# Performance work log

Hardware: AMD Instinct MI355X
Metric: run time of the kernel (lower is better)

The kernel has to match this reference:

```python
import jax, jax.numpy as jnp
import numpy as np

EMBED_DIM = 1024
NUM_HEADS = 16
HEAD_DIM = EMBED_DIM // NUM_HEADS
B, S = 2, 2048


def setup_inputs() -> dict:
    key = jax.random.key(0)
    ks = jax.random.split(key, 11)
    init = 0.02
    return {
        "query": jax.random.normal(ks[0], (B, S, EMBED_DIM), jnp.float32),
        "key": jax.random.normal(ks[1], (B, S, EMBED_DIM), jnp.float32),
        "value": jax.random.normal(ks[2], (B, S, EMBED_DIM), jnp.float32),
        "Wq": jax.random.normal(ks[3], (EMBED_DIM, EMBED_DIM), jnp.float32) * init,
        "bq": jnp.zeros((EMBED_DIM,), jnp.float32),
        "Wk": jax.random.normal(ks[4], (EMBED_DIM, EMBED_DIM), jnp.float32) * init,
        "bk": jnp.zeros((EMBED_DIM,), jnp.float32),
        "Wv": jax.random.normal(ks[5], (EMBED_DIM, EMBED_DIM), jnp.float32) * init,
        "bv": jnp.zeros((EMBED_DIM,), jnp.float32),
        "Wo": jax.random.normal(ks[6], (EMBED_DIM, EMBED_DIM), jnp.float32) * init,
        "bo": jnp.zeros((EMBED_DIM,), jnp.float32),
    }


def reference(query, key, value, Wq, bq, Wk, bk, Wv, bv, Wo, bo):
    scale = jnp.sqrt(jnp.asarray(HEAD_DIM, query.dtype))
    # projections (torch Linear: x @ W.T + b)
    Q = query @ Wq.T + bq
    K = key @ Wk.T + bk
    V = value @ Wv.T + bv
    # [B, S, E] -> [B, H, S, D]
    def split_heads(x):
        return x.reshape(B, -1, NUM_HEADS, HEAD_DIM).transpose(0, 2, 1, 3)
    Qh, Kh, Vh = split_heads(Q), split_heads(K), split_heads(V)
    # scores: [B, H, S, S] -- the O(N^2) intermediate
    scores = jnp.einsum("bhqd,bhkd->bhqk", Qh, Kh) / scale
    attn_weights = jax.nn.softmax(scores, axis=-1)
    # dropout = 0.0 (eval mode)
    out = jnp.einsum("bhqk,bhkd->bhqd", attn_weights, Vh)
    out = out.transpose(0, 2, 1, 3).reshape(B, -1, EMBED_DIM)
    output = out @ Wo.T + bo
    return output, attn_weights
```

## Files before the change

### kernel.cpp

```cpp
#include <hip/hip_runtime.h>
#include <hip/hip_bf16.h>

typedef unsigned short u16;
typedef u16 u16x8 __attribute__((ext_vector_type(8)));
typedef u16 u16x4 __attribute__((ext_vector_type(4)));
typedef __bf16 bf16x8 __attribute__((ext_vector_type(8)));
typedef float f32x4 __attribute__((ext_vector_type(4)));

#define B_ 2
#define S_ 2048
#define E_ 1024
#define H_ 16
#define D_ 64
#define QSCALE 0.18033688011112042f

__device__ __forceinline__ u16 f2bf(float f) {
    return __builtin_bit_cast(u16, static_cast<__bf16>(f));
}
__device__ __forceinline__ float bf2f(unsigned u) {
    return __builtin_bit_cast(float, u << 16);
}

__device__ __forceinline__ void glds16(const u16* g, u16* l) {
    __builtin_amdgcn_global_load_lds(
        (const __attribute__((address_space(1))) unsigned int*)g,
        (__attribute__((address_space(3))) unsigned int*)l, 16, 0, 0);
}

#define VMCNT0 asm volatile("s_waitcnt vmcnt(0)" ::: "memory")
#define RAW_BAR() do { __builtin_amdgcn_s_barrier(); asm volatile("" ::: "memory"); } while (0)

__device__ __forceinline__ bf16x8 lds_read8(const u16* base, int row, int k) {
    const char* p = (const char*)base + (((row * 128) + (k * 2)) ^ ((row & 7) << 4));
    return __builtin_bit_cast(bf16x8, *(const u16x8*)p);
}

__device__ __forceinline__ f32x4 mfma16x16(bf16x8 a, bf16x8 b, f32x4 c) {
    return __builtin_amdgcn_mfma_f32_16x16x32_bf16(a, b, c, 0, 0, 0);
}

__global__ __launch_bounds__(256) void cvt_kernel(const float* __restrict__ q,
                                                  const float* __restrict__ k,
                                                  const float* __restrict__ v,
                                                  const float* __restrict__ wq,
                                                  const float* __restrict__ wk,
                                                  const float* __restrict__ wv,
                                                  const float* __restrict__ wo,
                                                  u16* __restrict__ qkv_dst,
                                                  u16* __restrict__ w_dst) {
    const int bid = blockIdx.x;
    const float* src;
    u16* dst;
    if (bid < 6144) {
        const int t = bid >> 11, lb = bid & 2047;
        src = (t == 0 ? q : t == 1 ? k : v) + (size_t)lb * 2048;
        dst = qkv_dst + (size_t)t * 4194304 + (size_t)lb * 2048;
    } else {
        const int t = (bid - 6144) >> 9, lb = (bid - 6144) & 511;
        src = (t == 0 ? wq : t == 1 ? wk : t == 2 ? wv : wo) + (size_t)lb * 2048;
        dst = w_dst + (size_t)t * 1048576 + (size_t)lb * 2048;
    }
    const int off = threadIdx.x * 8;
    f32x4 a = *(const f32x4*)(src + off);
    f32x4 b = *(const f32x4*)(src + off + 4);
    u16x8 o;
#pragma unroll
    for (int i = 0; i < 4; ++i) { o[i] = f2bf(a[i]); o[4 + i] = f2bf(b[i]); }
    *(u16x8*)(dst + off) = o;
}

__global__ __launch_bounds__(256) void gemm_qkv(const u16* __restrict__ qkv_bf,
                                                const u16* __restrict__ w_bf,
                                                const float* __restrict__ bq,
                                                const float* __restrict__ bk,
                                                const float* __restrict__ bv,
                                                u16* __restrict__ outbase) {
    const int z = blockIdx.z;
    const u16* A = qkv_bf + (size_t)z * 4194304;
    const u16* W = w_bf + (size_t)z * 1048576;
    const float* bias = (z == 0) ? bq : (z == 1) ? bk : bv;
    u16* outp = outbase + (size_t)z * 4194304;

    const int n0 = blockIdx.x * 64;
    const int m0 = blockIdx.y * 128;
    const int tid = threadIdx.x;
    const int lane = tid & 63, g = lane >> 4, c = lane & 15;
    const int w = tid >> 6, wm = w >> 1, wn = w & 1;

    __shared__ u16 lA[2][8192];
    __shared__ u16 lB[2][4096];

    auto stage = [&](int buf, int kt) {
#pragma unroll
        for (int i = 0; i < 4; ++i) {
            const int chunk = (w * 4 + i) * 64 + lane;
            const int r = chunk >> 3, sg = chunk & 7, ss = sg ^ (r & 7);
            glds16(A + (size_t)(m0 + r) * 1024 + kt * 64 + ss * 8, &lA[buf][(w * 4 + i) * 512]);
        }
#pragma unroll
        for (int i = 0; i < 2; ++i) {
            const int chunk = (w * 2 + i) * 64 + lane;
            const int r = chunk >> 3, sg = chunk & 7, ss = sg ^ (r & 7);
            glds16(W + (size_t)(n0 + r) * 1024 + kt * 64 + ss * 8, &lB[buf][(w * 2 + i) * 512]);
        }
    };

    f32x4 acc[4][2] = {};
    stage(0, 0);
    VMCNT0;
    __syncthreads();

    for (int kt = 0; kt < 16; ++kt) {
        const int buf = kt & 1;
        if (kt < 15) stage(buf ^ 1, kt + 1);
#pragma unroll
        for (int ks = 0; ks < 2; ++ks) {
            bf16x8 af[4], bfr[2];
#pragma unroll
            for (int fm = 0; fm < 4; ++fm) af[fm] = lds_read8(lA[buf], wm * 64 + fm * 16 + c, g * 8 + ks * 32);
#pragma unroll
            for (int fn = 0; fn < 2; ++fn) bfr[fn] = lds_read8(lB[buf], wn * 32 + fn * 16 + c, g * 8 + ks * 32);
#pragma unroll
            for (int fm = 0; fm < 4; ++fm)
#pragma unroll
                for (int fn = 0; fn < 2; ++fn)
                    acc[fm][fn] = mfma16x16(af[fm], bfr[fn], acc[fm][fn]);
        }
        VMCNT0;
        RAW_BAR();
    }

    float bv_[2];
#pragma unroll
    for (int fn = 0; fn < 2; ++fn) bv_[fn] = bias[n0 + wn * 32 + fn * 16 + c];

#pragma unroll
    for (int fm = 0; fm < 4; ++fm) {
#pragma unroll
        for (int fn = 0; fn < 2; ++fn) {
            const int mbase = m0 + wm * 64 + fm * 16 + g * 4;
            const int n = n0 + wn * 32 + fn * 16 + c;
            if (z == 2) {
                u16x4 vv;
#pragma unroll
                for (int r = 0; r < 4; ++r) vv[r] = f2bf(acc[fm][fn][r] + bv_[fn]);
                const int b = mbase >> 11, s = mbase & 2047, h = n >> 6, d = n & 63;
                u16* dst = outp + ((size_t)((b * 16 + h) * 64 + d)) * 2048 + s;
                *(u16x4*)dst = vv;
            } else {
                const float sc = (z == 0) ? QSCALE : 1.0f;
#pragma unroll
                for (int r = 0; r < 4; ++r) {
                    const float val = (acc[fm][fn][r] + bv_[fn]) * sc;
                    const int m = mbase + r;
                    const int b = m >> 11, s = m & 2047, h = n >> 6, d = n & 63;
                    outp[((size_t)((b * 16 + h) * 2048 + s)) * 64 + d] = f2bf(val);
                }
            }
        }
    }
}

__global__ __launch_bounds__(256) void gemm_out(const u16* __restrict__ A,
                                                const u16* __restrict__ W,
                                                const float* __restrict__ bias,
                                                float* __restrict__ outp) {
    const int n0 = blockIdx.x * 64;
    const int m0 = blockIdx.y * 128;
    const int tid = threadIdx.x;
    const int lane = tid & 63, g = lane >> 4, c = lane & 15;
    const int w = tid >> 6, wm = w >> 1, wn = w & 1;

    __shared__ u16 lA[2][8192];
    __shared__ u16 lB[2][4096];

    auto stage = [&](int buf, int kt) {
#pragma unroll
        for (int i = 0; i < 4; ++i) {
            const int chunk = (w * 4 + i) * 64 + lane;
            const int r = chunk >> 3, sg = chunk & 7, ss = sg ^ (r & 7);
            glds16(A + (size_t)(m0 + r) * 1024 + kt * 64 + ss * 8, &lA[buf][(w * 4 + i) * 512]);
        }
#pragma unroll
        for (int i = 0; i < 2; ++i) {
            const int chunk = (w * 2 + i) * 64 + lane;
            const int r = chunk >> 3, sg = chunk & 7, ss = sg ^ (r & 7);
            glds16(W + (size_t)(n0 + r) * 1024 + kt * 64 + ss * 8, &lB[buf][(w * 2 + i) * 512]);
        }
    };

    f32x4 acc[4][2] = {};
    stage(0, 0);
    VMCNT0;
    __syncthreads();

    for (int kt = 0; kt < 16; ++kt) {
        const int buf = kt & 1;
        if (kt < 15) stage(buf ^ 1, kt + 1);
#pragma unroll
        for (int ks = 0; ks < 2; ++ks) {
            bf16x8 af[4], bfr[2];
#pragma unroll
            for (int fm = 0; fm < 4; ++fm) af[fm] = lds_read8(lA[buf], wm * 64 + fm * 16 + c, g * 8 + ks * 32);
#pragma unroll
            for (int fn = 0; fn < 2; ++fn) bfr[fn] = lds_read8(lB[buf], wn * 32 + fn * 16 + c, g * 8 + ks * 32);
#pragma unroll
            for (int fm = 0; fm < 4; ++fm)
#pragma unroll
                for (int fn = 0; fn < 2; ++fn)
                    acc[fm][fn] = mfma16x16(af[fm], bfr[fn], acc[fm][fn]);
        }
        VMCNT0;
        RAW_BAR();
    }

    float bv_[2];
#pragma unroll
    for (int fn = 0; fn < 2; ++fn) bv_[fn] = bias[n0 + wn * 32 + fn * 16 + c];

#pragma unroll
    for (int fm = 0; fm < 4; ++fm)
#pragma unroll
        for (int fn = 0; fn < 2; ++fn) {
            const int mbase = m0 + wm * 64 + fm * 16 + g * 4;
            const int n = n0 + wn * 32 + fn * 16 + c;
#pragma unroll
            for (int r = 0; r < 4; ++r)
                outp[(size_t)(mbase + r) * 1024 + n] = acc[fm][fn][r] + bv_[fn];
        }
}

__global__ __launch_bounds__(256) void attn_kernel(const u16* __restrict__ Qh,
                                                   const u16* __restrict__ Kh,
                                                   const u16* __restrict__ Vt,
                                                   float* __restrict__ attnW,
                                                   u16* __restrict__ Obf) {
    const int bid = blockIdx.x;
    const int sw = ((bid & 7) << 6) + (bid >> 3);
    const int bh = sw >> 4, qt = sw & 15;
    const int tid = threadIdx.x;
    const int lane = tid & 63, g = lane >> 4, c = lane & 15;
    const int w = tid >> 6;

    __shared__ u16 lQ[8192];
    __shared__ u16 lK[2][4096];
    __shared__ u16 lV[2][4096];
    __shared__ u16 lP[4][2048];

    const u16* Qbase = Qh + ((size_t)bh * S_ + qt * 128) * D_;
    const u16* Kbase = Kh + (size_t)bh * S_ * D_;
    const u16* Vbase = Vt + (size_t)bh * D_ * S_;

#pragma unroll
    for (int i = 0; i < 4; ++i) {
        const int chunk = (w * 4 + i) * 64 + lane;
        const int r = chunk >> 3, sg = chunk & 7, ss = sg ^ (r & 7);
        glds16(Qbase + r * 64 + ss * 8, &lQ[(w * 4 + i) * 512]);
    }
    auto stageK = [&](int buf, int kt) {
#pragma unroll
        for (int i = 0; i < 2; ++i) {
            const int chunk = (w * 2 + i) * 64 + lane;
            const int r = chunk >> 3, sg = chunk & 7, ss = sg ^ (r & 7);
            glds16(Kbase + (size_t)(kt * 64 + r) * 64 + ss * 8, &lK[buf][(w * 2 + i) * 512]);
        }
    };
    auto stageV = [&](int buf, int kt) {
#pragma unroll
        for (int i = 0; i < 2; ++i) {
            const int chunk = (w * 2 + i) * 64 + lane;
            const int r = chunk >> 3, sg = chunk & 7, ss = sg ^ (r & 7);
            glds16(Vbase + (size_t)r * S_ + kt * 64 + ss * 8, &lV[buf][(w * 2 + i) * 512]);
        }
    };

    stageK(0, 0);
    VMCNT0;
    __syncthreads();

    float l_run[2] = {0.f, 0.f};

    for (int kt = 0; kt < 32; ++kt) {
        const int buf = kt & 1;
        if (kt < 31) stageK(buf ^ 1, kt + 1);

        f32x4 s[4][2] = {};
        __builtin_amdgcn_s_setprio(1);
#pragma unroll
        for (int ks = 0; ks < 2; ++ks) {
            bf16x8 a[4], b[2];
#pragma unroll
            for (int kf = 0; kf < 4; ++kf) a[kf] = lds_read8(lK[buf], kf * 16 + c, g * 8 + ks * 32);
#pragma unroll
            for (int qf = 0; qf < 2; ++qf) b[qf] = lds_read8(lQ, w * 32 + qf * 16 + c, g * 8 + ks * 32);
#pragma unroll
            for (int kf = 0; kf < 4; ++kf)
#pragma unroll
                for (int qf = 0; qf < 2; ++qf)
                    s[kf][qf] = mfma16x16(a[kf], b[qf], s[kf][qf]);
        }
        __builtin_amdgcn_s_setprio(0);
#pragma unroll
        for (int qf = 0; qf < 2; ++qf) {
            float ts = 0.f;
#pragma unroll
            for (int kf = 0; kf < 4; ++kf)
#pragma unroll
                for (int r = 0; r < 4; ++r) ts += exp2f(s[kf][qf][r]);
            ts += __shfl_xor(ts, 16);
            ts += __shfl_xor(ts, 32);
            l_run[qf] += ts;
        }
        VMCNT0;
        RAW_BAR();
    }
    const float linv[2] = {1.f / l_run[0], 1.f / l_run[1]};

    f32x4 o[2][4] = {};
    stageK(0, 0);
    stageV(0, 0);
    VMCNT0;
    __syncthreads();

    for (int kt = 0; kt < 32; ++kt) {
        const int buf = kt & 1;
        if (kt < 31) { stageK(buf ^ 1, kt + 1); stageV(buf ^ 1, kt + 1); }

        f32x4 s[4][2] = {};
        __builtin_amdgcn_s_setprio(1);
#pragma unroll
        for (int ks = 0; ks < 2; ++ks) {
            bf16x8 a[4], b[2];
#pragma unroll
            for (int kf = 0; kf < 4; ++kf) a[kf] = lds_read8(lK[buf], kf * 16 + c, g * 8 + ks * 32);
#pragma unroll
            for (int qf = 0; qf < 2; ++qf) b[qf] = lds_read8(lQ, w * 32 + qf * 16 + c, g * 8 + ks * 32);
#pragma unroll
            for (int kf = 0; kf < 4; ++kf)
#pragma unroll
                for (int qf = 0; qf < 2; ++qf)
                    s[kf][qf] = mfma16x16(a[kf], b[qf], s[kf][qf]);
        }
        __builtin_amdgcn_s_setprio(0);

        u16* myP = lP[w];
#pragma unroll
        for (int qf = 0; qf < 2; ++qf) {
#pragma unroll
            for (int kf = 0; kf < 4; ++kf) {
                f32x4 p4;
#pragma unroll
                for (int r = 0; r < 4; ++r) p4[r] = exp2f(s[kf][qf][r]) * linv[qf];
#pragma unroll
                for (int rp = 0; rp < 2; ++rp) {
                    const unsigned pk = (unsigned)f2bf(p4[2 * rp]) |
                                        ((unsigned)f2bf(p4[2 * rp + 1]) << 16);
                    const int row = qf * 16 + c;
                    const int col = kf * 16 + g * 4 + 2 * rp;
                    *(unsigned*)((char*)myP + (((row * 128) + (col * 2)) ^ ((row & 7) << 4))) = pk;
                }
            }
        }

        __builtin_amdgcn_s_setprio(1);
#pragma unroll
        for (int ks = 0; ks < 2; ++ks) {
            bf16x8 pa[2], vb[4];
#pragma unroll
            for (int fm = 0; fm < 2; ++fm) pa[fm] = lds_read8(myP, fm * 16 + c, g * 8 + ks * 32);
#pragma unroll
            for (int fn = 0; fn < 4; ++fn) vb[fn] = lds_read8(lV[buf], fn * 16 + c, g * 8 + ks * 32);
#pragma unroll
            for (int fm = 0; fm < 2; ++fm)
#pragma unroll
                for (int fn = 0; fn < 4; ++fn)
                    o[fm][fn] = mfma16x16(pa[fm], vb[fn], o[fm][fn]);
        }
        __builtin_amdgcn_s_setprio(0);

        {
            const size_t qbase = (size_t)bh * S_ + (size_t)(qt * 128 + w * 32);
#pragma unroll
            for (int j = 0; j < 8; ++j) {
                const int row = j * 4 + g;
                const unsigned long long pv8 = *(const unsigned long long*)(
                    (const char*)myP + (((row * 128) + c * 8) ^ ((row & 7) << 4)));
                f32x4 o4;
                o4[0] = bf2f((unsigned)(pv8 & 0xffffu));
                o4[1] = bf2f((unsigned)((pv8 >> 16) & 0xffffu));
                o4[2] = bf2f((unsigned)((pv8 >> 32) & 0xffffu));
                o4[3] = bf2f((unsigned)((pv8 >> 48) & 0xffffu));
                __builtin_nontemporal_store(
                    o4, (f32x4*)(attnW + (qbase + row) * S_ + kt * 64 + c * 4));
            }
        }

        asm volatile("s_waitcnt vmcnt(8)" ::: "memory");
        RAW_BAR();
    }

    const int b2 = bh >> 4, h = bh & 15;
#pragma unroll
    for (int fm = 0; fm < 2; ++fm)
#pragma unroll
        for (int fn = 0; fn < 4; ++fn)
#pragma unroll
            for (int r = 0; r < 4; ++r) {
                const int q = qt * 128 + w * 32 + fm * 16 + g * 4 + r;
                const int d = fn * 16 + c;
                Obf[((size_t)(b2 * S_ + q)) * E_ + h * 64 + d] = f2bf(o[fm][fn][r]);
            }
}

extern "C" void kernel_launch(void* const* d_in, const int* in_sizes, int n_in,
                              void* d_out, int out_size, void* d_ws, size_t ws_size,
                              hipStream_t stream) {
    const float* query = (const float*)d_in[0];
    const float* key_ = (const float*)d_in[1];
    const float* value = (const float*)d_in[2];
    const float* Wq = (const float*)d_in[3];
    const float* bq = (const float*)d_in[4];
    const float* Wk = (const float*)d_in[5];
    const float* bk = (const float*)d_in[6];
    const float* Wv = (const float*)d_in[7];
    const float* bv = (const float*)d_in[8];
    const float* Wo = (const float*)d_in[9];
    const float* bo = (const float*)d_in[10];

    u16* qkv_bf = (u16*)d_ws;
    u16* w_bf = qkv_bf + (size_t)12 * 1024 * 1024;
    u16* Qh = qkv_bf + (size_t)16 * 1024 * 1024;
    u16* Obf = qkv_bf;

    float* out0 = (float*)d_out;
    float* attnW = out0 + (size_t)B_ * S_ * E_;

    cvt_kernel<<<8192, 256, 0, stream>>>(query, key_, value, Wq, Wk, Wv, Wo, qkv_bf, w_bf);

    gemm_qkv<<<dim3(16, 32, 3), 256, 0, stream>>>(qkv_bf, w_bf, bq, bk, bv, Qh);

    attn_kernel<<<512, 256, 0, stream>>>(Qh, Qh + (size_t)4 * 1024 * 1024,
                                         Qh + (size_t)8 * 1024 * 1024, attnW, Obf);

    gemm_out<<<dim3(16, 32), 256, 0, stream>>>(Obf, w_bf + (size_t)3 * 1024 * 1024, bo, (float*)d_out);
}
```

Baseline: 234.9 us.

## Enlarge GEMM tiles to 128x128 and stage 128-key tiles in attention pass one

Both projection GEMMs now use 128x128 output tiles with a 4x4 MFMA accumulator grid per wave, which halves the grid and reuses each A tile across twice as many columns. In the attention kernel the K and V buffers are merged into one shared array. The row-sum pass now stages 128 keys per barrier and processes them as two 64-key sub-blocks, which halves the number of sync points in that pass. The attention output stores become nontemporal. The trade-off is higher register and LDS use per block and fewer blocks in the GEMMs (768 and 256), which may lower occupancy.

```diff
diff --git a/kernel.cpp b/kernel.cpp
--- a/kernel.cpp
+++ b/kernel.cpp
@@ -81,14 +81,14 @@
     const float* bias = (z == 0) ? bq : (z == 1) ? bk : bv;
     u16* outp = outbase + (size_t)z * 4194304;
 
-    const int n0 = blockIdx.x * 64;
+    const int n0 = blockIdx.x * 128;
     const int m0 = blockIdx.y * 128;
     const int tid = threadIdx.x;
     const int lane = tid & 63, g = lane >> 4, c = lane & 15;
     const int w = tid >> 6, wm = w >> 1, wn = w & 1;
 
     __shared__ u16 lA[2][8192];
-    __shared__ u16 lB[2][4096];
+    __shared__ u16 lB[2][8192];
 
     auto stage = [&](int buf, int kt) {
 #pragma unroll
@@ -96,16 +96,11 @@
             const int chunk = (w * 4 + i) * 64 + lane;
             const int r = chunk >> 3, sg = chunk & 7, ss = sg ^ (r & 7);
             glds16(A + (size_t)(m0 + r) * 1024 + kt * 64 + ss * 8, &lA[buf][(w * 4 + i) * 512]);
-        }
-#pragma unroll
-        for (int i = 0; i < 2; ++i) {
-            const int chunk = (w * 2 + i) * 64 + lane;
-            const int r = chunk >> 3, sg = chunk & 7, ss = sg ^ (r & 7);
-            glds16(W + (size_t)(n0 + r) * 1024 + kt * 64 + ss * 8, &lB[buf][(w * 2 + i) * 512]);
+            glds16(W + (size_t)(n0 + r) * 1024 + kt * 64 + ss * 8, &lB[buf][(w * 4 + i) * 512]);
         }
     };
 
-    f32x4 acc[4][2] = {};
+    f32x4 acc[4][4] = {};
     stage(0, 0);
     VMCNT0;
     __syncthreads();
@@ -115,31 +110,31 @@
         if (kt < 15) stage(buf ^ 1, kt + 1);
 #pragma unroll
         for (int ks = 0; ks < 2; ++ks) {
-            bf16x8 af[4], bfr[2];
+            bf16x8 af[4], bfr[4];
 #pragma unroll
             for (int fm = 0; fm < 4; ++fm) af[fm] = lds_read8(lA[buf], wm * 64 + fm * 16 + c, g * 8 + ks * 32);
 #pragma unroll
-            for (int fn = 0; fn < 2; ++fn) bfr[fn] = lds_read8(lB[buf], wn * 32 + fn * 16 + c, g * 8 + ks * 32);
+            for (int fn = 0; fn < 4; ++fn) bfr[fn] = lds_read8(lB[buf], wn * 64 + fn * 16 + c, g * 8 + ks * 32);
 #pragma unroll
             for (int fm = 0; fm < 4; ++fm)
 #pragma unroll
-                for (int fn = 0; fn < 2; ++fn)
+                for (int fn = 0; fn < 4; ++fn)
                     acc[fm][fn] = mfma16x16(af[fm], bfr[fn], acc[fm][fn]);
         }
         VMCNT0;
         RAW_BAR();
     }
 
-    float bv_[2];
-#pragma unroll
-    for (int fn = 0; fn < 2; ++fn) bv_[fn] = bias[n0 + wn * 32 + fn * 16 + c];
+    float bv_[4];
+#pragma unroll
+    for (int fn = 0; fn < 4; ++fn) bv_[fn] = bias[n0 + wn * 64 + fn * 16 + c];
 
 #pragma unroll
     for (int fm = 0; fm < 4; ++fm) {
 #pragma unroll
-        for (int fn = 0; fn < 2; ++fn) {
+        for (int fn = 0; fn < 4; ++fn) {
             const int mbase = m0 + wm * 64 + fm * 16 + g * 4;
-            const int n = n0 + wn * 32 + fn * 16 + c;
+            const int n = n0 + wn * 64 + fn * 16 + c;
             if (z == 2) {
                 u16x4 vv;
 #pragma unroll
@@ -165,14 +160,14 @@
                                                 const u16* __restrict__ W,
                                                 const float* __restrict__ bias,
                                                 float* __restrict__ outp) {
-    const int n0 = blockIdx.x * 64;
+    const int n0 = blockIdx.x * 128;
     const int m0 = blockIdx.y * 128;
     const int tid = threadIdx.x;
     const int lane = tid & 63, g = lane >> 4, c = lane & 15;
     const int w = tid >> 6, wm = w >> 1, wn = w & 1;
 
     __shared__ u16 lA[2][8192];
-    __shared__ u16 lB[2][4096];
+    __shared__ u16 lB[2][8192];
 
     auto stage = [&](int buf, int kt) {
 #pragma unroll
@@ -180,16 +175,11 @@
             const int chunk = (w * 4 + i) * 64 + lane;
             const int r = chunk >> 3, sg = chunk & 7, ss = sg ^ (r & 7);
             glds16(A + (size_t)(m0 + r) * 1024 + kt * 64 + ss * 8, &lA[buf][(w * 4 + i) * 512]);
-        }
-#pragma unroll
-        for (int i = 0; i < 2; ++i) {
-            const int chunk = (w * 2 + i) * 64 + lane;
-            const int r = chunk >> 3, sg = chunk & 7, ss = sg ^ (r & 7);
-            glds16(W + (size_t)(n0 + r) * 1024 + kt * 64 + ss * 8, &lB[buf][(w * 2 + i) * 512]);
+            glds16(W + (size_t)(n0 + r) * 1024 + kt * 64 + ss * 8, &lB[buf][(w * 4 + i) * 512]);
         }
     };
 
-    f32x4 acc[4][2] = {};
+    f32x4 acc[4][4] = {};
     stage(0, 0);
     VMCNT0;
     __syncthreads();
@@ -199,31 +189,31 @@
         if (kt < 15) stage(buf ^ 1, kt + 1);
 #pragma unroll
         for (int ks = 0; ks < 2; ++ks) {
-            bf16x8 af[4], bfr[2];
+            bf16x8 af[4], bfr[4];
 #pragma unroll
             for (int fm = 0; fm < 4; ++fm) af[fm] = lds_read8(lA[buf], wm * 64 + fm * 16 + c, g * 8 + ks * 32);
 #pragma unroll
-            for (int fn = 0; fn < 2; ++fn) bfr[fn] = lds_read8(lB[buf], wn * 32 + fn * 16 + c, g * 8 + ks * 32);
+            for (int fn = 0; fn < 4; ++fn) bfr[fn] = lds_read8(lB[buf], wn * 64 + fn * 16 + c, g * 8 + ks * 32);
 #pragma unroll
             for (int fm = 0; fm < 4; ++fm)
 #pragma unroll
-                for (int fn = 0; fn < 2; ++fn)
+                for (int fn = 0; fn < 4; ++fn)
                     acc[fm][fn] = mfma16x16(af[fm], bfr[fn], acc[fm][fn]);
         }
         VMCNT0;
         RAW_BAR();
     }
 
-    float bv_[2];
-#pragma unroll
-    for (int fn = 0; fn < 2; ++fn) bv_[fn] = bias[n0 + wn * 32 + fn * 16 + c];
+    float bv_[4];
+#pragma unroll
+    for (int fn = 0; fn < 4; ++fn) bv_[fn] = bias[n0 + wn * 64 + fn * 16 + c];
 
 #pragma unroll
     for (int fm = 0; fm < 4; ++fm)
 #pragma unroll
-        for (int fn = 0; fn < 2; ++fn) {
+        for (int fn = 0; fn < 4; ++fn) {
             const int mbase = m0 + wm * 64 + fm * 16 + g * 4;
-            const int n = n0 + wn * 32 + fn * 16 + c;
+            const int n = n0 + wn * 64 + fn * 16 + c;
 #pragma unroll
             for (int r = 0; r < 4; ++r)
                 outp[(size_t)(mbase + r) * 1024 + n] = acc[fm][fn][r] + bv_[fn];
@@ -243,8 +233,7 @@
     const int w = tid >> 6;
 
     __shared__ u16 lQ[8192];
-    __shared__ u16 lK[2][4096];
-    __shared__ u16 lV[2][4096];
+    __shared__ u16 lKV[2][8192];
     __shared__ u16 lP[4][2048];
 
     const u16* Qbase = Qh + ((size_t)bh * S_ + qt * 128) * D_;
@@ -257,32 +246,77 @@
         const int r = chunk >> 3, sg = chunk & 7, ss = sg ^ (r & 7);
         glds16(Qbase + r * 64 + ss * 8, &lQ[(w * 4 + i) * 512]);
     }
-    auto stageK = [&](int buf, int kt) {
+    auto stageK128 = [&](int buf, int kt2) {
+#pragma unroll
+        for (int i = 0; i < 4; ++i) {
+            const int chunk = (w * 4 + i) * 64 + lane;
+            const int r = chunk >> 3, sg = chunk & 7, ss = sg ^ (r & 7);
+            glds16(Kbase + (size_t)(kt2 * 128 + r) * 64 + ss * 8, &lKV[buf][(w * 4 + i) * 512]);
+        }
+    };
+    auto stageKV64 = [&](int buf, int kt) {
 #pragma unroll
         for (int i = 0; i < 2; ++i) {
             const int chunk = (w * 2 + i) * 64 + lane;
             const int r = chunk >> 3, sg = chunk & 7, ss = sg ^ (r & 7);
-            glds16(Kbase + (size_t)(kt * 64 + r) * 64 + ss * 8, &lK[buf][(w * 2 + i) * 512]);
+            glds16(Kbase + (size_t)(kt * 64 + r) * 64 + ss * 8, &lKV[buf][(w * 2 + i) * 512]);
+            glds16(Vbase + (size_t)r * S_ + kt * 64 + ss * 8, &lKV[buf][4096 + (w * 2 + i) * 512]);
         }
     };
-    auto stageV = [&](int buf, int kt) {
-#pragma unroll
-        for (int i = 0; i < 2; ++i) {
-            const int chunk = (w * 2 + i) * 64 + lane;
-            const int r = chunk >> 3, sg = chunk & 7, ss = sg ^ (r & 7);
-            glds16(Vbase + (size_t)r * S_ + kt * 64 + ss * 8, &lV[buf][(w * 2 + i) * 512]);
-        }
-    };
-
-    stageK(0, 0);
+
+    stageK128(0, 0);
     VMCNT0;
     __syncthreads();
 
     float l_run[2] = {0.f, 0.f};
 
+    for (int kt2 = 0; kt2 < 16; ++kt2) {
+        const int buf = kt2 & 1;
+        if (kt2 < 15) stageK128(buf ^ 1, kt2 + 1);
+
+#pragma unroll
+        for (int sub = 0; sub < 2; ++sub) {
+            f32x4 s[4][2] = {};
+            __builtin_amdgcn_s_setprio(1);
+#pragma unroll
+            for (int ks = 0; ks < 2; ++ks) {
+                bf16x8 a[4], b[2];
+#pragma unroll
+                for (int kf = 0; kf < 4; ++kf) a[kf] = lds_read8(lKV[buf], sub * 64 + kf * 16 + c, g * 8 + ks * 32);
+#pragma unroll
+                for (int qf = 0; qf < 2; ++qf) b[qf] = lds_read8(lQ, w * 32 + qf * 16 + c, g * 8 + ks * 32);
+#pragma unroll
+                for (int kf = 0; kf < 4; ++kf)
+#pragma unroll
+                    for (int qf = 0; qf < 2; ++qf)
+                        s[kf][qf] = mfma16x16(a[kf], b[qf], s[kf][qf]);
+            }
+            __builtin_amdgcn_s_setprio(0);
+#pragma unroll
+            for (int qf = 0; qf < 2; ++qf) {
+                float ts = 0.f;
+#pragma unroll
+                for (int kf = 0; kf < 4; ++kf)
+#pragma unroll
+                    for (int r = 0; r < 4; ++r) ts += exp2f(s[kf][qf][r]);
+                ts += __shfl_xor(ts, 16);
+                ts += __shfl_xor(ts, 32);
+                l_run[qf] += ts;
+            }
+        }
+        VMCNT0;
+        RAW_BAR();
+    }
+    const float linv[2] = {1.f / l_run[0], 1.f / l_run[1]};
+
+    f32x4 o[2][4] = {};
+    stageKV64(0, 0);
+    VMCNT0;
+    RAW_BAR();
+
     for (int kt = 0; kt < 32; ++kt) {
         const int buf = kt & 1;
-        if (kt < 31) stageK(buf ^ 1, kt + 1);
+        if (kt < 31) stageKV64(buf ^ 1, kt + 1);
 
         f32x4 s[4][2] = {};
         __builtin_amdgcn_s_setprio(1);
@@ -290,49 +324,7 @@
         for (int ks = 0; ks < 2; ++ks) {
             bf16x8 a[4], b[2];
 #pragma unroll
-            for (int kf = 0; kf < 4; ++kf) a[kf] = lds_read8(lK[buf], kf * 16 + c, g * 8 + ks * 32);
-#pragma unroll
-            for (int qf = 0; qf < 2; ++qf) b[qf] = lds_read8(lQ, w * 32 + qf * 16 + c, g * 8 + ks * 32);
-#pragma unroll
-            for (int kf = 0; kf < 4; ++kf)
-#pragma unroll
-                for (int qf = 0; qf < 2; ++qf)
-                    s[kf][qf] = mfma16x16(a[kf], b[qf], s[kf][qf]);
-        }
-        __builtin_amdgcn_s_setprio(0);
-#pragma unroll
-        for (int qf = 0; qf < 2; ++qf) {
-            float ts = 0.f;
-#pragma unroll
-            for (int kf = 0; kf < 4; ++kf)
-#pragma unroll
-                for (int r = 0; r < 4; ++r) ts += exp2f(s[kf][qf][r]);
-            ts += __shfl_xor(ts, 16);
-            ts += __shfl_xor(ts, 32);
-            l_run[qf] += ts;
-        }
-        VMCNT0;
-        RAW_BAR();
-    }
-    const float linv[2] = {1.f / l_run[0], 1.f / l_run[1]};
-
-    f32x4 o[2][4] = {};
-    stageK(0, 0);
-    stageV(0, 0);
-    VMCNT0;
-    __syncthreads();
-
-    for (int kt = 0; kt < 32; ++kt) {
-        const int buf = kt & 1;
-        if (kt < 31) { stageK(buf ^ 1, kt + 1); stageV(buf ^ 1, kt + 1); }
-
-        f32x4 s[4][2] = {};
-        __builtin_amdgcn_s_setprio(1);
-#pragma unroll
-        for (int ks = 0; ks < 2; ++ks) {
-            bf16x8 a[4], b[2];
-#pragma unroll
-            for (int kf = 0; kf < 4; ++kf) a[kf] = lds_read8(lK[buf], kf * 16 + c, g * 8 + ks * 32);
+            for (int kf = 0; kf < 4; ++kf) a[kf] = lds_read8(lKV[buf], kf * 16 + c, g * 8 + ks * 32);
 #pragma unroll
             for (int qf = 0; qf < 2; ++qf) b[qf] = lds_read8(lQ, w * 32 + qf * 16 + c, g * 8 + ks * 32);
 #pragma unroll
@@ -369,7 +361,7 @@
 #pragma unroll
             for (int fm = 0; fm < 2; ++fm) pa[fm] = lds_read8(myP, fm * 16 + c, g * 8 + ks * 32);
 #pragma unroll
-            for (int fn = 0; fn < 4; ++fn) vb[fn] = lds_read8(lV[buf], fn * 16 + c, g * 8 + ks * 32);
+            for (int fn = 0; fn < 4; ++fn) vb[fn] = lds_read8(lKV[buf] + 4096, fn * 16 + c, g * 8 + ks * 32);
 #pragma unroll
             for (int fm = 0; fm < 2; ++fm)
 #pragma unroll
@@ -408,7 +400,9 @@
             for (int r = 0; r < 4; ++r) {
                 const int q = qt * 128 + w * 32 + fm * 16 + g * 4 + r;
                 const int d = fn * 16 + c;
-                Obf[((size_t)(b2 * S_ + q)) * E_ + h * 64 + d] = f2bf(o[fm][fn][r]);
+                __builtin_nontemporal_store(
+                    f2bf(o[fm][fn][r]),
+                    &Obf[((size_t)(b2 * S_ + q)) * E_ + h * 64 + d]);
             }
 }
 
@@ -437,10 +431,10 @@
 
     cvt_kernel<<<8192, 256, 0, stream>>>(query, key_, value, Wq, Wk, Wv, Wo, qkv_bf, w_bf);
 
-    gemm_qkv<<<dim3(16, 32, 3), 256, 0, stream>>>(qkv_bf, w_bf, bq, bk, bv, Qh);
+    gemm_qkv<<<dim3(8, 32, 3), 256, 0, stream>>>(qkv_bf, w_bf, bq, bk, bv, Qh);
 
     attn_kernel<<<512, 256, 0, stream>>>(Qh, Qh + (size_t)4 * 1024 * 1024,
                                          Qh + (size_t)8 * 1024 * 1024, attnW, Obf);
 
-    gemm_out<<<dim3(16, 32), 256, 0, stream>>>(Obf, w_bf + (size_t)3 * 1024 * 1024, bo, (float*)d_out);
-}
+    gemm_out<<<dim3(8, 32), 256, 0, stream>>>(Obf, w_bf + (size_t)3 * 1024 * 1024, bo, (float*)d_out);
+}
```

Result: no change. 234.0 us (-0.4%).
